# Kernel tuning notes

Measured on AMD Instinct MI355X. Metric: run time of the kernel, lower is better.

The kernel has to match this reference:

```python
import jax, jax.numpy as jnp
import numpy as np

DIM = 1024
B, S = 16, 2048

def setup_inputs() -> dict:
    key = jax.random.key(0)
    ks = jax.random.split(key, 8)
    scale = 1.0 / np.sqrt(DIM)
    x = jax.random.normal(ks[0], (B, S, DIM), dtype=jnp.float32)
    mask = jax.random.randint(ks[1], (B, S), 0, 2, dtype=jnp.int32)
    Wq = jax.random.normal(ks[2], (DIM, DIM), dtype=jnp.float32) * scale
    Wk = jax.random.normal(ks[3], (DIM, DIM), dtype=jnp.float32) * scale
    Wv = jax.random.normal(ks[4], (DIM, DIM), dtype=jnp.float32) * scale
    bq = jax.random.normal(ks[5], (DIM,), dtype=jnp.float32) * 0.01
    bk = jax.random.normal(ks[6], (DIM,), dtype=jnp.float32) * 0.01
    bv = jax.random.normal(ks[7], (DIM,), dtype=jnp.float32) * 0.01
    return {"x": x, "mask": mask, "Wq": Wq, "bq": bq, "Wk": Wk, "bk": bk, "Wv": Wv, "bv": bv}

def reference(x, mask, Wq, bq, Wk, bk, Wv, bv):
    # Q/K/V projections (torch Linear: x @ W.T + b)
    Q = jnp.einsum('bsd,ed->bse', x, Wq) + bq
    K = jnp.einsum('bsd,ed->bse', x, Wk) + bk
    V = jnp.einsum('bsd,ed->bse', x, Wv) + bv
    inv_sqrt_d = 1.0 / jnp.sqrt(jnp.asarray(x.shape[-1], dtype=x.dtype))
    scores = jnp.einsum('bqd,bkd->bqk', Q, K) * inv_sqrt_d  # [B,S,S]
    # mask: [B,S] -> broadcast over query dim; 0 = padding -> -inf
    scores = jnp.where(mask[:, None, :] == 0, -jnp.inf, scores)
    attn = jax.nn.softmax(scores, axis=-1)
    attn = jnp.nan_to_num(attn, nan=0.0)  # rows fully masked -> 0 (matches torch)
    out = jnp.einsum('bqk,bkd->bqd', attn, V)
    return out.mean(axis=1)  # [B, DIM]
```

## Files before the change

kernel.cpp:

```cpp
#include <hip/hip_runtime.h>
#include <hip/hip_bf16.h>
#include <stdint.h>

#define NBATCH 16
#define SEQ    2048
#define DMODEL 1024
#define KSPLIT 16

#define CS      0.03125f
#define KSC     3.0517578125e-5f
#define NEG4LN2 2.772588722f

typedef __attribute__((ext_vector_type(8))) short short8;
typedef __attribute__((ext_vector_type(4))) float f32x4;
typedef __attribute__((ext_vector_type(4))) int i32x4;
typedef __attribute__((ext_vector_type(16))) int i32x16;

struct __align__(8) bf4 { __hip_bfloat16 h[4]; };

__device__ __forceinline__ float bf2f(short s) {
  union { uint32_t u; float f; } c;
  c.u = ((uint32_t)(uint16_t)s) << 16;
  return c.f;
}
__device__ __forceinline__ int qs8(float f, float sc) {
  int v = __float2int_rn(f * sc);
  return v > 127 ? 127 : (v < -127 ? -127 : v);
}

__device__ __forceinline__ void gload16(const void* g, void* l) {
  __builtin_amdgcn_global_load_lds(
      (const __attribute__((address_space(1))) void*)g,
      (__attribute__((address_space(3))) void*)l, 16, 0, 0);
}

#define BAR() __builtin_amdgcn_s_barrier()
#define WAIT_LGKM0()                                         \
  do {                                                       \
    asm volatile("s_waitcnt lgkmcnt(0)" ::: "memory");       \
    __builtin_amdgcn_sched_barrier(0);                       \
  } while (0)
#define WAIT_VM0()                                           \
  do {                                                       \
    asm volatile("s_waitcnt vmcnt(0)" ::: "memory");         \
  } while (0)

template <int TP>
__global__ __launch_bounds__(512, 2)
void gemmT_kernel(const __hip_bfloat16* __restrict__ Aall,
                  const __hip_bfloat16* __restrict__ Ball,
                  uint8_t* __restrict__ O8, int ldo) {
  __shared__ __align__(16) char smem[131072];
  const int t = threadIdx.x, lane = t & 63, wid = t >> 6;
  const int wm = wid >> 2, wn = wid & 3;
  const int g = lane >> 4, l15 = lane & 15, l7 = lane & 7;

  const int at2base = blockIdx.x * TP;
  const int bt2 = blockIdx.y;
  const __hip_bfloat16* Bb = Ball + (size_t)bt2 * 256 * DMODEL;
  auto Aof = [&](int tp) { return Aall + (size_t)(at2base + tp) * 256 * DMODEL; };

  const int srl = t >> 3;
  const int sc8 = (t & 7) ^ (srl & 7);
  const int pc8[2] = {g ^ l7, (4 + g) ^ l7};

  auto stage_mat = [&](const __hip_bfloat16* gs, char* dst, int kt) {
#pragma unroll
    for (int it = 0; it < 4; ++it)
      gload16(gs + (size_t)(it * 64 + srl) * DMODEL + kt * 64 + sc8 * 8,
              dst + it * 8192 + wid * 1024);
  };

  f32x4 acc[8][4];
#pragma unroll
  for (int m = 0; m < 8; ++m)
#pragma unroll
    for (int n = 0; n < 4; ++n) acc[m][n] = (f32x4){0.f, 0.f, 0.f, 0.f};
  short8 afr[2][4], bfr[2][2][2];

#define LDA_Q(MH)                                                           \
  { _Pragma("unroll") for (int m = 0; m < 4; ++m) {                         \
      const int row = wm * 128 + ((MH) * 4 + m) * 16 + l15;                 \
      afr[0][m] = *(const short8*)(At + row * 128 + pc8[0] * 16);           \
      afr[1][m] = *(const short8*)(At + row * 128 + pc8[1] * 16);           \
    } }
#define LDB_Q(NH)                                                           \
  { _Pragma("unroll") for (int n = 0; n < 2; ++n) {                         \
      const int row = wn * 64 + ((NH) * 2 + n) * 16 + l15;                  \
      bfr[NH][0][n] = *(const short8*)(Bt + row * 128 + pc8[0] * 16);       \
      bfr[NH][1][n] = *(const short8*)(Bt + row * 128 + pc8[1] * 16);       \
    } }
#define MFMA_Q(MH, NH)                                                      \
  { __builtin_amdgcn_s_setprio(1);                                          \
    _Pragma("unroll") for (int kk = 0; kk < 2; ++kk)                        \
    _Pragma("unroll") for (int m = 0; m < 4; ++m)                           \
    _Pragma("unroll") for (int n = 0; n < 2; ++n)                           \
      acc[(MH)*4+m][(NH)*2+n] = __builtin_amdgcn_mfma_f32_16x16x32_bf16(    \
          afr[kk][m], bfr[NH][kk][n], acc[(MH)*4+m][(NH)*2+n], 0, 0, 0);    \
    __builtin_amdgcn_s_setprio(0); }

  auto EPI = [&](int at2) {
    const size_t orow0 = (size_t)bt2 * 256 + wn * 64 + l15;
    const int ocol0 = at2 * 256 + wm * 128 + g * 4;
#pragma unroll
    for (int mi = 0; mi < 8; ++mi)
#pragma unroll
      for (int ni = 0; ni < 4; ++ni) {
        uint32_t pk = 0;
#pragma unroll
        for (int j = 0; j < 4; ++j)
          pk |= (uint32_t)(qs8(acc[mi][ni][j], 1024.f) & 0xff) << (8 * j);
        *(uint32_t*)(O8 + (orow0 + ni * 16) * (size_t)ldo + ocol0 + mi * 16) = pk;
      }
#pragma unroll
    for (int m = 0; m < 8; ++m)
#pragma unroll
      for (int n = 0; n < 4; ++n) acc[m][n] = (f32x4){0.f, 0.f, 0.f, 0.f};
  };

  stage_mat(Aof(0), smem, 0);
  stage_mat(Bb, smem + 32768, 0);
  WAIT_VM0();
  BAR();

  const int NI = 16 * TP;
#pragma unroll 1
  for (int ii = 0; ii < NI; ++ii) {
    const int p = ii & 1;
    const char* At = smem + (p << 16);
    const char* Bt = smem + 32768 + (p << 16);
    char* An = smem + ((p ^ 1) << 16);
    char* Bn = smem + 32768 + ((p ^ 1) << 16);
    const int kn = (ii + 1) & 15;
    LDA_Q(0) LDB_Q(0)
    if (ii + 1 < NI) stage_mat(Aof((ii + 1) >> 4), An, kn);
    BAR(); WAIT_LGKM0(); MFMA_Q(0, 0) BAR();
    LDB_Q(1)
    if (ii + 1 < NI) stage_mat(Bb, Bn, kn);
    BAR(); WAIT_LGKM0(); MFMA_Q(0, 1) BAR();
    LDA_Q(1)
    BAR(); WAIT_LGKM0(); MFMA_Q(1, 0) BAR();
    MFMA_Q(1, 1)
    WAIT_VM0();
    if ((ii & 15) == 15) EPI(at2base + (ii >> 4));
    BAR();
  }
#undef LDA_Q
#undef LDB_Q
#undef MFMA_Q
}

template <int MODE, int TP>
__global__ __launch_bounds__(1024)
void i8gemm_kernel(const uint8_t* __restrict__ Aall,
                   const uint8_t* __restrict__ Ball,
                   uint8_t* __restrict__ OUT8,
                   const float* __restrict__ vball,
                   float* __restrict__ Zpart, int b0) {
  __shared__ __align__(16) char smem[131072 + 4096];
  const int t = threadIdx.x, lane = t & 63, wid = t >> 6;
  const int wm = wid >> 2, wn = wid & 3;
  const int l31 = lane & 31, half = lane >> 5, l7 = lane & 7;

  int at2base, bt2, cb = 0, b = 0;
  const uint8_t *Bb, *Abatch;
  if constexpr (MODE == 0) {
    at2base = blockIdx.x * TP;
    bt2 = blockIdx.y;
    Abatch = Aall;
    Bb = Ball + (size_t)bt2 * 256 * DMODEL;
  } else {
    cb = blockIdx.y; b = b0 + cb;
    bt2 = blockIdx.x & 7;
    at2base = (blockIdx.x >> 3) * TP;
    Abatch = Aall + (size_t)b * SEQ * DMODEL;
    Bb = Ball + ((size_t)b * SEQ + bt2 * 256) * DMODEL;
  }
  auto Aof = [&](int tp) { return Abatch + (size_t)(at2base + tp) * 256 * DMODEL; };

  const int sc8 = (t & 7) ^ ((t >> 3) & 7);
  int pcI[4];
#pragma unroll
  for (int ks = 0; ks < 4; ++ks) pcI[ks] = ((ks * 2 + half) ^ l7) * 16;

  auto stage_mat = [&](const uint8_t* gs, char* dst, int kt) {
#pragma unroll
    for (int it = 0; it < 2; ++it)
      gload16(gs + (size_t)(it * 128 + (t >> 3)) * DMODEL + kt * 128 + sc8 * 16,
              dst + it * 16384 + wid * 1024);
  };

  i32x16 acci[2][2];
#pragma unroll
  for (int m = 0; m < 2; ++m)
#pragma unroll
    for (int n = 0; n < 2; ++n)
#pragma unroll
      for (int r = 0; r < 16; ++r) acci[m][n][r] = 0;

  auto EPI = [&](int at2) {
    if constexpr (MODE == 0) {
#pragma unroll
      for (int mt = 0; mt < 2; ++mt) {
        const int arow_base = at2 * 256 + wm * 64 + mt * 32 + 4 * half;
#pragma unroll
        for (int nt = 0; nt < 2; ++nt) {
          const int bcol = bt2 * 256 + wn * 64 + nt * 32 + l31;
#pragma unroll
          for (int r = 0; r < 16; ++r) {
            const int arow = arow_base + (r & 3) + 8 * (r >> 2);
            OUT8[(size_t)arow * DMODEL + bcol] =
                (uint8_t)qs8((float)acci[mt][nt][r], 9.765625e-4f);
          }
        }
      }
    } else {
      float zc[2] = {0.f, 0.f};
#pragma unroll
      for (int mt = 0; mt < 2; ++mt) {
        const int krow_base = at2 * 256 + wm * 64 + mt * 32 + 4 * half;
        float4 vv[4];
#pragma unroll
        for (int gg = 0; gg < 4; ++gg)
          vv[gg] = *(const float4*)&vball[(size_t)b * SEQ + krow_base + 8 * gg];
#pragma unroll
        for (int nt = 0; nt < 2; ++nt) {
          const int qcol = bt2 * 256 + wn * 64 + nt * 32 + l31;
#pragma unroll
          for (int r = 0; r < 16; r += 2) {
            const float vj0 = ((const float*)&vv[r >> 2])[r & 3];
            const float vj1 = ((const float*)&vv[r >> 2])[(r + 1) & 3];
            const float e0 = __expf(fmaf((float)acci[mt][nt][r], KSC, vj0));
            const float e1 = __expf(fmaf((float)acci[mt][nt][r + 1], KSC, vj1));
            zc[nt] += e0 + e1;
            const unsigned p = __builtin_amdgcn_cvt_pk_fp8_f32(e0, e1, 0, false);
            const int krow = krow_base + (r & 3) + 8 * (r >> 2);
            uint8_t* ad = OUT8 + ((size_t)cb * SEQ + krow) * (size_t)SEQ + qcol;
            ad[0] = (uint8_t)p;
            ad[SEQ] = (uint8_t)(p >> 8);
          }
        }
      }
#pragma unroll
      for (int nt = 0; nt < 2; ++nt) {
        float v = zc[nt];
        v += __shfl_xor(v, 32);
        zc[nt] = v;
      }
      float* red = (float*)(smem + 131072);
      if (lane < 32) {
#pragma unroll
        for (int nt = 0; nt < 2; ++nt)
          red[wm * 256 + wn * 64 + nt * 32 + l31] = zc[nt];
      }
      __syncthreads();
      if (t < 256)
        Zpart[((size_t)cb * 8 + at2) * SEQ + bt2 * 256 + t] =
            red[t] + red[256 + t] + red[512 + t] + red[768 + t];
    }
#pragma unroll
    for (int m = 0; m < 2; ++m)
#pragma unroll
      for (int n = 0; n < 2; ++n)
#pragma unroll
        for (int r = 0; r < 16; ++r) acci[m][n][r] = 0;
  };

  stage_mat(Aof(0), smem, 0);
  stage_mat(Bb, smem + 32768, 0);
  WAIT_VM0();
  BAR();

  const int NI = 8 * TP;
#pragma unroll 1
  for (int ii = 0; ii < NI; ++ii) {
    const int p = ii & 1;
    const char* Al = smem + (p << 16);
    const char* Bl = smem + 32768 + (p << 16);
    if (ii + 1 < NI) {
      stage_mat(Aof((ii + 1) >> 3), smem + ((p ^ 1) << 16), (ii + 1) & 7);
      stage_mat(Bb, smem + 32768 + ((p ^ 1) << 16), (ii + 1) & 7);
    }
    const int rA0 = (wm * 64 + l31) * 128, rA1 = (wm * 64 + 32 + l31) * 128;
    const int rB0 = (wn * 64 + l31) * 128, rB1 = (wn * 64 + 32 + l31) * 128;
#pragma unroll
    for (int ks = 0; ks < 4; ++ks) {
      const i32x4 af0 = *(const i32x4*)(Al + rA0 + pcI[ks]);
      const i32x4 af1 = *(const i32x4*)(Al + rA1 + pcI[ks]);
      const i32x4 bf0 = *(const i32x4*)(Bl + rB0 + pcI[ks]);
      const i32x4 bf1 = *(const i32x4*)(Bl + rB1 + pcI[ks]);
      __builtin_amdgcn_s_setprio(1);
      acci[0][0] = __builtin_amdgcn_mfma_i32_32x32x32_i8(af0, bf0, acci[0][0], 0, 0, 0);
      acci[0][1] = __builtin_amdgcn_mfma_i32_32x32x32_i8(af0, bf1, acci[0][1], 0, 0, 0);
      acci[1][0] = __builtin_amdgcn_mfma_i32_32x32x32_i8(af1, bf0, acci[1][0], 0, 0, 0);
      acci[1][1] = __builtin_amdgcn_mfma_i32_32x32x32_i8(af1, bf1, acci[1][1], 0, 0, 0);
      __builtin_amdgcn_s_setprio(0);
    }
    WAIT_LGKM0();
    WAIT_VM0();
    if ((ii & 7) == 7) EPI(at2base + (ii >> 3));
    BAR();
  }
}

__global__ void transpose_cvt_kernel(const float* __restrict__ in,
                                     __hip_bfloat16* __restrict__ outp) {
  __shared__ float tile[32][33];
  const int bx = blockIdx.x, by = blockIdx.y;
  const int tx = threadIdx.x & 31, ty = threadIdx.x >> 5;
#pragma unroll
  for (int r = 0; r < 32; r += 8)
    tile[ty + r][tx] = in[(size_t)(by * 32 + ty + r) * DMODEL + bx * 32 + tx];
  __syncthreads();
#pragma unroll
  for (int r = 0; r < 32; r += 8)
    outp[(size_t)(bx * 32 + ty + r) * DMODEL + by * 32 + tx] =
        __float2bfloat16(tile[tx][ty + r]);
}

__global__ __launch_bounds__(256)
void prep_t2_kernel(const __hip_bfloat16* __restrict__ WkT,
                    const float* __restrict__ bq, float* __restrict__ t2) {
  const int wave = threadIdx.x >> 6, lane = threadIdx.x & 63;
  const int d = blockIdx.x * 4 + wave;
  const short8* kr = (const short8*)(WkT + (size_t)d * DMODEL);
  float a2 = 0.f;
#pragma unroll
  for (int h = 0; h < 2; ++h) {
    const short8 kv = kr[lane * 2 + h];
    const int e0 = lane * 16 + h * 8;
#pragma unroll
    for (int i = 0; i < 8; ++i) a2 += bf2f(kv[i]) * bq[e0 + i];
  }
  a2 += __shfl_down(a2, 32); a2 += __shfl_down(a2, 16); a2 += __shfl_down(a2, 8);
  a2 += __shfl_down(a2, 4);  a2 += __shfl_down(a2, 2);  a2 += __shfl_down(a2, 1);
  if (lane == 0) t2[d] = a2;
}

__global__ __launch_bounds__(256)
void cvtv_kernel(const float* __restrict__ x, const float* __restrict__ t2,
                 const int* __restrict__ mask,
                 uint8_t* __restrict__ x8, float* __restrict__ vb) {
  const int wave = threadIdx.x >> 6, lane = threadIdx.x & 63;
  const size_t row = (size_t)blockIdx.x * 4 + wave;
  const float* xr = x + row * DMODEL;
  float a2 = 0.f;
#pragma unroll
  for (int p = 0; p < 4; ++p) {
    const int d = p * 256 + lane * 4;
    const float4 xv = *(const float4*)(xr + d);
    const float4 tv = *(const float4*)(t2 + d);
    a2 += xv.x * tv.x + xv.y * tv.y + xv.z * tv.z + xv.w * tv.w;
    uint32_t qp = (uint32_t)(qs8(xv.x, 32.f) & 0xff) |
                  ((uint32_t)(qs8(xv.y, 32.f) & 0xff) << 8) |
                  ((uint32_t)(qs8(xv.z, 32.f) & 0xff) << 16) |
                  ((uint32_t)(qs8(xv.w, 32.f) & 0xff) << 24);
    *(uint32_t*)(x8 + row * DMODEL + d) = qp;
  }
  a2 += __shfl_down(a2, 32); a2 += __shfl_down(a2, 16); a2 += __shfl_down(a2, 8);
  a2 += __shfl_down(a2, 4);  a2 += __shfl_down(a2, 2);  a2 += __shfl_down(a2, 1);
  if (lane == 0)
    vb[row] = mask[row] ? fmaf(a2, CS, -NEG4LN2) : -1e30f;
}

__global__ void zinv_kernel(const float* __restrict__ Zpart,
                            float* __restrict__ rZ, int n) {
  const int idx = blockIdx.x * 256 + threadIdx.x;
  if (idx >= n) return;
  const int cb = idx >> 11, q = idx & (SEQ - 1);
  float z = 0.f;
#pragma unroll
  for (int kt = 0; kt < 8; ++kt)
    z += Zpart[((size_t)cb * 8 + kt) * SEQ + q];
  rZ[(size_t)cb * SEQ + q] = (z > 0.f) ? (1.f / z) : 0.f;
}

__global__ __launch_bounds__(256)
void passB_kernel(const uint8_t* __restrict__ E8,
                  const float* __restrict__ rZ,
                  float* __restrict__ wout) {
  const int t = threadIdx.x, lane = t & 63, wave = t >> 6;
  const int cb = blockIdx.y;
  float4 rzv[4][2];
#pragma unroll
  for (int it = 0; it < 4; ++it) {
    const float4* p = (const float4*)(rZ + (size_t)cb * SEQ + it * 512 + lane * 8);
    rzv[it][0] = p[0];
    rzv[it][1] = p[1];
  }
  const int kbase = blockIdx.x * 16 + wave * 4;
#pragma unroll
  for (int r = 0; r < 4; ++r) {
    const int k = kbase + r;
    const uint2* Ep = (const uint2*)(E8 + ((size_t)cb * SEQ + k) * SEQ);
    float s = 0.f;
#pragma unroll
    for (int it = 0; it < 4; ++it) {
      const uint2 v = Ep[it * 64 + lane];
      const float* rz = (const float*)&rzv[it][0];
      s += __builtin_amdgcn_cvt_f32_fp8(v.x, 0) * rz[0];
      s += __builtin_amdgcn_cvt_f32_fp8(v.x, 1) * rz[1];
      s += __builtin_amdgcn_cvt_f32_fp8(v.x, 2) * rz[2];
      s += __builtin_amdgcn_cvt_f32_fp8(v.x, 3) * rz[3];
      s += __builtin_amdgcn_cvt_f32_fp8(v.y, 0) * rz[4];
      s += __builtin_amdgcn_cvt_f32_fp8(v.y, 1) * rz[5];
      s += __builtin_amdgcn_cvt_f32_fp8(v.y, 2) * rz[6];
      s += __builtin_amdgcn_cvt_f32_fp8(v.y, 3) * rz[7];
    }
    s += __shfl_down(s, 32); s += __shfl_down(s, 16); s += __shfl_down(s, 8);
    s += __shfl_down(s, 4);  s += __shfl_down(s, 2);  s += __shfl_down(s, 1);
    if (lane == 0) wout[(size_t)cb * SEQ + k] = s;
  }
}

__global__ void sumw_kernel(const float* __restrict__ w,
                            float* __restrict__ sumw_all, int b0) {
  __shared__ float sred[4];
  const int t = threadIdx.x, lane = t & 63, wave = t >> 6;
  const int cb = blockIdx.x;
  float v = 0.f;
  for (int k = t; k < SEQ; k += 256) v += w[(size_t)cb * SEQ + k];
  v += __shfl_down(v, 32); v += __shfl_down(v, 16); v += __shfl_down(v, 8);
  v += __shfl_down(v, 4);  v += __shfl_down(v, 2);  v += __shfl_down(v, 1);
  if (lane == 0) sred[wave] = v;
  __syncthreads();
  if (t == 0) sumw_all[b0 + cb] = sred[0] + sred[1] + sred[2] + sred[3];
}

__global__ __launch_bounds__(256)
void wxpart_kernel(const uint8_t* __restrict__ x8,
                   const float* __restrict__ w,
                   float* __restrict__ wxp, int b0) {
  const int cb = blockIdx.y, kq = blockIdx.z;
  const int b = b0 + cb;
  const int d4 = threadIdx.x;
  const uint8_t* xb =
      x8 + ((size_t)b * SEQ + (size_t)kq * (SEQ / KSPLIT)) * DMODEL;
  const float* wb = w + (size_t)cb * SEQ + (size_t)kq * (SEQ / KSPLIT);
  float a0 = 0.f, a1 = 0.f, a2 = 0.f, a3 = 0.f;
#pragma unroll 4
  for (int k = 0; k < SEQ / KSPLIT; ++k) {
    const float wk = wb[k];
    const uint32_t pv = *(const uint32_t*)(xb + (size_t)k * DMODEL + d4 * 4);
    a0 += wk * (float)(int8_t)(pv & 0xff);
    a1 += wk * (float)(int8_t)((pv >> 8) & 0xff);
    a2 += wk * (float)(int8_t)((pv >> 16) & 0xff);
    a3 += wk * (float)(int8_t)(pv >> 24);
  }
  float4* o = (float4*)&wxp[((size_t)kq * NBATCH + b) * DMODEL + d4 * 4];
  *o = make_float4(a0 * 0.03125f, a1 * 0.03125f, a2 * 0.03125f, a3 * 0.03125f);
}

__global__ void final_kernel(const float* __restrict__ wxp,
                             const float* __restrict__ sumw_all,
                             const float* __restrict__ Wv,
                             const float* __restrict__ bv,
                             float* __restrict__ out) {
  const int b = blockIdx.y, eg = blockIdx.x;
  const int wave = threadIdx.x >> 6, lane = threadIdx.x & 63;
  const int e = eg * 4 + wave;
  float acc = 0.f;
  for (int d = lane; d < DMODEL; d += 64) {
    float wx = 0.f;
#pragma unroll
    for (int kq = 0; kq < KSPLIT; ++kq)
      wx += wxp[((size_t)kq * NBATCH + b) * DMODEL + d];
    acc += wx * Wv[(size_t)e * DMODEL + d];
  }
  acc += __shfl_down(acc, 32); acc += __shfl_down(acc, 16);
  acc += __shfl_down(acc, 8);  acc += __shfl_down(acc, 4);
  acc += __shfl_down(acc, 2);  acc += __shfl_down(acc, 1);
  if (lane == 0)
    out[(size_t)b * DMODEL + e] =
        (acc + sumw_all[b] * bv[e]) * (1.f / (float)SEQ);
}

extern "C" void kernel_launch(void* const* d_in, const int* in_sizes, int n_in,
                              void* d_out, int out_size, void* d_ws, size_t ws_size,
                              hipStream_t stream) {
  const float* x  = (const float*)d_in[0];
  const int* mask = (const int*)d_in[1];
  const float* Wq = (const float*)d_in[2];
  const float* bq = (const float*)d_in[3];
  const float* Wk = (const float*)d_in[4];
  const float* bk = (const float*)d_in[5];
  const float* Wv = (const float*)d_in[6];
  const float* bv = (const float*)d_in[7];
  float* out = (float*)d_out;
  (void)bk;

  char* ws = (char*)d_ws;
  size_t off = 0;
  auto alloc = [&](size_t bytes) -> void* {
    void* p = ws + off;
    off += (bytes + 255) & ~(size_t)255;
    return p;
  };
  uint8_t* Mt8 = (uint8_t*)alloc((size_t)DMODEL * DMODEL);
  __hip_bfloat16* WqT_bf = (__hip_bfloat16*)alloc((size_t)DMODEL * DMODEL * 2);
  __hip_bfloat16* WkT_bf = (__hip_bfloat16*)alloc((size_t)DMODEL * DMODEL * 2);
  float* wxp      = (float*)alloc((size_t)KSPLIT * NBATCH * DMODEL * 4);
  float* sumw_all = (float*)alloc((size_t)NBATCH * 4);
  float* t2       = (float*)alloc((size_t)DMODEL * 4);
  uint8_t* x8i = (uint8_t*)alloc((size_t)NBATCH * SEQ * DMODEL);
  uint8_t* Y8i = (uint8_t*)alloc((size_t)NBATCH * SEQ * DMODEL);
  float* vb = (float*)alloc((size_t)NBATCH * SEQ * 4);
  const size_t fixed = off;

  const size_t per_batch = (size_t)SEQ * SEQ
                         + (size_t)8 * SEQ * 4
                         + (size_t)2 * SEQ * 4 + 8 * 256;
  long avail = (long)ws_size - (long)fixed;
  int NB = (int)(avail / (long)per_batch);
  if (NB < 1) NB = 1;
  if (NB > NBATCH) NB = NBATCH;
  while (NBATCH % NB) --NB;
  uint8_t* Ebuf = (uint8_t*)alloc((size_t)NB * SEQ * SEQ);
  float* Zpart = (float*)alloc((size_t)NB * 8 * SEQ * 4);
  float* rZ    = (float*)alloc((size_t)NB * SEQ * 4);
  float* wbuf  = (float*)alloc((size_t)NB * SEQ * 4);

  transpose_cvt_kernel<<<dim3(32, 32), dim3(256), 0, stream>>>(Wq, WqT_bf);
  transpose_cvt_kernel<<<dim3(32, 32), dim3(256), 0, stream>>>(Wk, WkT_bf);
  gemmT_kernel<1><<<dim3(4, 4), dim3(512), 0, stream>>>(
      WqT_bf, WkT_bf, Mt8, DMODEL);
  prep_t2_kernel<<<dim3(256), dim3(256), 0, stream>>>(WkT_bf, bq, t2);
  cvtv_kernel<<<dim3(NBATCH * SEQ / 4), dim3(256), 0, stream>>>(
      x, t2, mask, x8i, vb);
  i8gemm_kernel<0, 2><<<dim3(64, DMODEL / 256), dim3(1024), 0, stream>>>(
      x8i, Mt8, Y8i, nullptr, nullptr, 0);

  for (int b0 = 0; b0 < NBATCH; b0 += NB) {
    const int nb = NB;
    i8gemm_kernel<1, 4><<<dim3(16, nb), dim3(1024), 0, stream>>>(
        x8i, Y8i, Ebuf, vb, Zpart, b0);
    zinv_kernel<<<dim3((nb * SEQ + 255) / 256), dim3(256), 0, stream>>>(
        Zpart, rZ, nb * SEQ);
    passB_kernel<<<dim3(SEQ / 16, nb), dim3(256), 0, stream>>>(Ebuf, rZ, wbuf);
    sumw_kernel<<<dim3(nb), dim3(256), 0, stream>>>(wbuf, sumw_all, b0);
    wxpart_kernel<<<dim3(1, nb, KSPLIT), dim3(256), 0, stream>>>(
        x8i, wbuf, wxp, b0);
  }
  final_kernel<<<dim3(DMODEL / 4, NBATCH), dim3(256), 0, stream>>>(
      wxp, sumw_all, Wv, bv, out);
}
```

Before: 277.6 us.

## Triple-buffer int8 GEMM staging and fuse softmax normalization kernels

```diff
diff --git a/kernel.cpp b/kernel.cpp
--- a/kernel.cpp
+++ b/kernel.cpp
@@ -43,6 +43,10 @@
 #define WAIT_VM0()                                           \
   do {                                                       \
     asm volatile("s_waitcnt vmcnt(0)" ::: "memory");         \
+  } while (0)
+#define WAIT_VM2()                                           \
+  do {                                                       \
+    asm volatile("s_waitcnt vmcnt(2)" ::: "memory");         \
   } while (0)
 
 template <int TP>
@@ -157,10 +161,10 @@
                    uint8_t* __restrict__ OUT8,
                    const float* __restrict__ vball,
                    float* __restrict__ Zpart, int b0) {
-  __shared__ __align__(16) char smem[131072 + 4096];
+  __shared__ __align__(16) char smem[98304 + 4096];
   const int t = threadIdx.x, lane = t & 63, wid = t >> 6;
   const int wm = wid >> 2, wn = wid & 3;
-  const int l31 = lane & 31, half = lane >> 5, l7 = lane & 7;
+  const int l31 = lane & 31, half = lane >> 5;
 
   int at2base, bt2, cb = 0, b = 0;
   const uint8_t *Bb, *Abatch;
@@ -178,17 +182,18 @@
   }
   auto Aof = [&](int tp) { return Abatch + (size_t)(at2base + tp) * 256 * DMODEL; };
 
-  const int sc8 = (t & 7) ^ ((t >> 3) & 7);
-  int pcI[4];
-#pragma unroll
-  for (int ks = 0; ks < 4; ++ks) pcI[ks] = ((ks * 2 + half) ^ l7) * 16;
-
-  auto stage_mat = [&](const uint8_t* gs, char* dst, int kt) {
-#pragma unroll
-    for (int it = 0; it < 2; ++it)
-      gload16(gs + (size_t)(it * 128 + (t >> 3)) * DMODEL + kt * 128 + sc8 * 16,
-              dst + it * 16384 + wid * 1024);
+  const int srow = t >> 2;
+  const int sc4 = (t & 3) ^ ((t >> 3) & 3);
+  auto stage_pair = [&](const uint8_t* ga, int kt, char* base) {
+    gload16(ga + (size_t)srow * DMODEL + kt * 64 + sc4 * 16, base + wid * 1024);
+    gload16(Bb + (size_t)srow * DMODEL + kt * 64 + sc4 * 16,
+            base + 16384 + wid * 1024);
   };
+
+  int pc4[2];
+#pragma unroll
+  for (int ks = 0; ks < 2; ++ks)
+    pc4[ks] = ((ks * 2 + half) ^ ((l31 >> 1) & 3)) * 16;
 
   i32x16 acci[2][2];
 #pragma unroll
@@ -247,7 +252,7 @@
         v += __shfl_xor(v, 32);
         zc[nt] = v;
       }
-      float* red = (float*)(smem + 131072);
+      float* red = (float*)(smem + 98304);
       if (lane < 32) {
 #pragma unroll
         for (int nt = 0; nt < 2; ++nt)
@@ -266,29 +271,27 @@
         for (int r = 0; r < 16; ++r) acci[m][n][r] = 0;
   };
 
-  stage_mat(Aof(0), smem, 0);
-  stage_mat(Bb, smem + 32768, 0);
-  WAIT_VM0();
+  const int NI = 16 * TP;
+  stage_pair(Aof(0), 0, smem);
+  if (NI > 1) stage_pair(Aof(1 >> 4), 1, smem + 32768);
+  WAIT_VM2();
   BAR();
 
-  const int NI = 8 * TP;
 #pragma unroll 1
-  for (int ii = 0; ii < NI; ++ii) {
-    const int p = ii & 1;
-    const char* Al = smem + (p << 16);
-    const char* Bl = smem + 32768 + (p << 16);
-    if (ii + 1 < NI) {
-      stage_mat(Aof((ii + 1) >> 3), smem + ((p ^ 1) << 16), (ii + 1) & 7);
-      stage_mat(Bb, smem + 32768 + ((p ^ 1) << 16), (ii + 1) & 7);
-    }
-    const int rA0 = (wm * 64 + l31) * 128, rA1 = (wm * 64 + 32 + l31) * 128;
-    const int rB0 = (wn * 64 + l31) * 128, rB1 = (wn * 64 + 32 + l31) * 128;
-#pragma unroll
-    for (int ks = 0; ks < 4; ++ks) {
-      const i32x4 af0 = *(const i32x4*)(Al + rA0 + pcI[ks]);
-      const i32x4 af1 = *(const i32x4*)(Al + rA1 + pcI[ks]);
-      const i32x4 bf0 = *(const i32x4*)(Bl + rB0 + pcI[ks]);
-      const i32x4 bf1 = *(const i32x4*)(Bl + rB1 + pcI[ks]);
+  for (int j = 0; j < NI; ++j) {
+    char* bcur = smem + (j % 3) * 32768;
+    if (j + 2 < NI)
+      stage_pair(Aof((j + 2) >> 4), (j + 2) & 15, smem + ((j + 2) % 3) * 32768);
+    const int rA0 = (wm * 64 + l31) * 64, rA1 = (wm * 64 + 32 + l31) * 64;
+    const int rB0 = (wn * 64 + l31) * 64, rB1 = (wn * 64 + 32 + l31) * 64;
+    const char* Al = bcur;
+    const char* Bl = bcur + 16384;
+#pragma unroll
+    for (int ks = 0; ks < 2; ++ks) {
+      const i32x4 af0 = *(const i32x4*)(Al + rA0 + pc4[ks]);
+      const i32x4 af1 = *(const i32x4*)(Al + rA1 + pc4[ks]);
+      const i32x4 bf0 = *(const i32x4*)(Bl + rB0 + pc4[ks]);
+      const i32x4 bf1 = *(const i32x4*)(Bl + rB1 + pc4[ks]);
       __builtin_amdgcn_s_setprio(1);
       acci[0][0] = __builtin_amdgcn_mfma_i32_32x32x32_i8(af0, bf0, acci[0][0], 0, 0, 0);
       acci[0][1] = __builtin_amdgcn_mfma_i32_32x32x32_i8(af0, bf1, acci[0][1], 0, 0, 0);
@@ -297,15 +300,20 @@
       __builtin_amdgcn_s_setprio(0);
     }
     WAIT_LGKM0();
-    WAIT_VM0();
-    if ((ii & 7) == 7) EPI(at2base + (ii >> 3));
+    if (j + 2 < NI) { WAIT_VM2(); }
+    else           { WAIT_VM0(); }
+    if ((j & 15) == 15) EPI(at2base + (j >> 4));
     BAR();
   }
 }
 
-__global__ void transpose_cvt_kernel(const float* __restrict__ in,
-                                     __hip_bfloat16* __restrict__ outp) {
+__global__ void transpose_cvt_kernel(const float* __restrict__ inq,
+                                     const float* __restrict__ ink,
+                                     __hip_bfloat16* __restrict__ outq,
+                                     __hip_bfloat16* __restrict__ outk) {
   __shared__ float tile[32][33];
+  const float* in = blockIdx.z ? ink : inq;
+  __hip_bfloat16* outp = blockIdx.z ? outk : outq;
   const int bx = blockIdx.x, by = blockIdx.y;
   const int tx = threadIdx.x & 31, ty = threadIdx.x >> 5;
 #pragma unroll
@@ -363,68 +371,58 @@
     vb[row] = mask[row] ? fmaf(a2, CS, -NEG4LN2) : -1e30f;
 }
 
-__global__ void zinv_kernel(const float* __restrict__ Zpart,
-                            float* __restrict__ rZ, int n) {
-  const int idx = blockIdx.x * 256 + threadIdx.x;
-  if (idx >= n) return;
-  const int cb = idx >> 11, q = idx & (SEQ - 1);
-  float z = 0.f;
-#pragma unroll
-  for (int kt = 0; kt < 8; ++kt)
-    z += Zpart[((size_t)cb * 8 + kt) * SEQ + q];
-  rZ[(size_t)cb * SEQ + q] = (z > 0.f) ? (1.f / z) : 0.f;
-}
-
 __global__ __launch_bounds__(256)
-void passB_kernel(const uint8_t* __restrict__ E8,
-                  const float* __restrict__ rZ,
-                  float* __restrict__ wout) {
+void wsolve_kernel(const uint8_t* __restrict__ E8,
+                   const float* __restrict__ Zpart,
+                   float* __restrict__ wout, float* __restrict__ sumwp,
+                   int b0) {
+  __shared__ float rz[SEQ];
+  __shared__ float sred[4];
   const int t = threadIdx.x, lane = t & 63, wave = t >> 6;
   const int cb = blockIdx.y;
+  for (int q = t; q < SEQ; q += 256) {
+    float z = 0.f;
+#pragma unroll
+    for (int kt = 0; kt < 8; ++kt)
+      z += Zpart[((size_t)cb * 8 + kt) * SEQ + q];
+    rz[q] = (z > 0.f) ? (1.f / z) : 0.f;
+  }
+  __syncthreads();
   float4 rzv[4][2];
 #pragma unroll
   for (int it = 0; it < 4; ++it) {
-    const float4* p = (const float4*)(rZ + (size_t)cb * SEQ + it * 512 + lane * 8);
-    rzv[it][0] = p[0];
-    rzv[it][1] = p[1];
-  }
-  const int kbase = blockIdx.x * 16 + wave * 4;
-#pragma unroll
-  for (int r = 0; r < 4; ++r) {
+    rzv[it][0] = *(const float4*)&rz[it * 512 + lane * 8];
+    rzv[it][1] = *(const float4*)&rz[it * 512 + lane * 8 + 4];
+  }
+  const int kbase = blockIdx.x * 128 + wave * 32;
+  float wsum = 0.f;
+#pragma unroll 1
+  for (int r = 0; r < 32; ++r) {
     const int k = kbase + r;
     const uint2* Ep = (const uint2*)(E8 + ((size_t)cb * SEQ + k) * SEQ);
     float s = 0.f;
 #pragma unroll
     for (int it = 0; it < 4; ++it) {
       const uint2 v = Ep[it * 64 + lane];
-      const float* rz = (const float*)&rzv[it][0];
-      s += __builtin_amdgcn_cvt_f32_fp8(v.x, 0) * rz[0];
-      s += __builtin_amdgcn_cvt_f32_fp8(v.x, 1) * rz[1];
-      s += __builtin_amdgcn_cvt_f32_fp8(v.x, 2) * rz[2];
-      s += __builtin_amdgcn_cvt_f32_fp8(v.x, 3) * rz[3];
-      s += __builtin_amdgcn_cvt_f32_fp8(v.y, 0) * rz[4];
-      s += __builtin_amdgcn_cvt_f32_fp8(v.y, 1) * rz[5];
-      s += __builtin_amdgcn_cvt_f32_fp8(v.y, 2) * rz[6];
-      s += __builtin_amdgcn_cvt_f32_fp8(v.y, 3) * rz[7];
+      const float* rzp = (const float*)&rzv[it][0];
+      s += __builtin_amdgcn_cvt_f32_fp8(v.x, 0) * rzp[0];
+      s += __builtin_amdgcn_cvt_f32_fp8(v.x, 1) * rzp[1];
+      s += __builtin_amdgcn_cvt_f32_fp8(v.x, 2) * rzp[2];
+      s += __builtin_amdgcn_cvt_f32_fp8(v.x, 3) * rzp[3];
+      s += __builtin_amdgcn_cvt_f32_fp8(v.y, 0) * rzp[4];
+      s += __builtin_amdgcn_cvt_f32_fp8(v.y, 1) * rzp[5];
+      s += __builtin_amdgcn_cvt_f32_fp8(v.y, 2) * rzp[6];
+      s += __builtin_amdgcn_cvt_f32_fp8(v.y, 3) * rzp[7];
     }
     s += __shfl_down(s, 32); s += __shfl_down(s, 16); s += __shfl_down(s, 8);
     s += __shfl_down(s, 4);  s += __shfl_down(s, 2);  s += __shfl_down(s, 1);
-    if (lane == 0) wout[(size_t)cb * SEQ + k] = s;
-  }
-}
-
-__global__ void sumw_kernel(const float* __restrict__ w,
-                            float* __restrict__ sumw_all, int b0) {
-  __shared__ float sred[4];
-  const int t = threadIdx.x, lane = t & 63, wave = t >> 6;
-  const int cb = blockIdx.x;
-  float v = 0.f;
-  for (int k = t; k < SEQ; k += 256) v += w[(size_t)cb * SEQ + k];
-  v += __shfl_down(v, 32); v += __shfl_down(v, 16); v += __shfl_down(v, 8);
-  v += __shfl_down(v, 4);  v += __shfl_down(v, 2);  v += __shfl_down(v, 1);
-  if (lane == 0) sred[wave] = v;
+    if (lane == 0) { wout[(size_t)cb * SEQ + k] = s; wsum += s; }
+  }
+  if (lane == 0) sred[wave] = wsum;
   __syncthreads();
-  if (t == 0) sumw_all[b0 + cb] = sred[0] + sred[1] + sred[2] + sred[3];
+  if (t == 0)
+    sumwp[(b0 + cb) * 16 + blockIdx.x] =
+        sred[0] + sred[1] + sred[2] + sred[3];
 }
 
 __global__ __launch_bounds__(256)
@@ -452,7 +450,7 @@
 }
 
 __global__ void final_kernel(const float* __restrict__ wxp,
-                             const float* __restrict__ sumw_all,
+                             const float* __restrict__ sumwp,
                              const float* __restrict__ Wv,
                              const float* __restrict__ bv,
                              float* __restrict__ out) {
@@ -470,9 +468,12 @@
   acc += __shfl_down(acc, 32); acc += __shfl_down(acc, 16);
   acc += __shfl_down(acc, 8);  acc += __shfl_down(acc, 4);
   acc += __shfl_down(acc, 2);  acc += __shfl_down(acc, 1);
-  if (lane == 0)
-    out[(size_t)b * DMODEL + e] =
-        (acc + sumw_all[b] * bv[e]) * (1.f / (float)SEQ);
+  if (lane == 0) {
+    float sw = 0.f;
+#pragma unroll
+    for (int i = 0; i < 16; ++i) sw += sumwp[b * 16 + i];
+    out[(size_t)b * DMODEL + e] = (acc + sw * bv[e]) * (1.f / (float)SEQ);
+  }
 }
 
 extern "C" void kernel_launch(void* const* d_in, const int* in_sizes, int n_in,
@@ -499,9 +500,9 @@
   uint8_t* Mt8 = (uint8_t*)alloc((size_t)DMODEL * DMODEL);
   __hip_bfloat16* WqT_bf = (__hip_bfloat16*)alloc((size_t)DMODEL * DMODEL * 2);
   __hip_bfloat16* WkT_bf = (__hip_bfloat16*)alloc((size_t)DMODEL * DMODEL * 2);
-  float* wxp      = (float*)alloc((size_t)KSPLIT * NBATCH * DMODEL * 4);
-  float* sumw_all = (float*)alloc((size_t)NBATCH * 4);
-  float* t2       = (float*)alloc((size_t)DMODEL * 4);
+  float* wxp   = (float*)alloc((size_t)KSPLIT * NBATCH * DMODEL * 4);
+  float* sumwp = (float*)alloc((size_t)NBATCH * 16 * 4);
+  float* t2    = (float*)alloc((size_t)DMODEL * 4);
   uint8_t* x8i = (uint8_t*)alloc((size_t)NBATCH * SEQ * DMODEL);
   uint8_t* Y8i = (uint8_t*)alloc((size_t)NBATCH * SEQ * DMODEL);
   float* vb = (float*)alloc((size_t)NBATCH * SEQ * 4);
@@ -509,7 +510,7 @@
 
   const size_t per_batch = (size_t)SEQ * SEQ
                          + (size_t)8 * SEQ * 4
-                         + (size_t)2 * SEQ * 4 + 8 * 256;
+                         + (size_t)SEQ * 4 + 8 * 256;
   long avail = (long)ws_size - (long)fixed;
   int NB = (int)(avail / (long)per_batch);
   if (NB < 1) NB = 1;
@@ -517,11 +518,10 @@
   while (NBATCH % NB) --NB;
   uint8_t* Ebuf = (uint8_t*)alloc((size_t)NB * SEQ * SEQ);
   float* Zpart = (float*)alloc((size_t)NB * 8 * SEQ * 4);
-  float* rZ    = (float*)alloc((size_t)NB * SEQ * 4);
   float* wbuf  = (float*)alloc((size_t)NB * SEQ * 4);
 
-  transpose_cvt_kernel<<<dim3(32, 32), dim3(256), 0, stream>>>(Wq, WqT_bf);
-  transpose_cvt_kernel<<<dim3(32, 32), dim3(256), 0, stream>>>(Wk, WkT_bf);
+  transpose_cvt_kernel<<<dim3(32, 32, 2), dim3(256), 0, stream>>>(
+      Wq, Wk, WqT_bf, WkT_bf);
   gemmT_kernel<1><<<dim3(4, 4), dim3(512), 0, stream>>>(
       WqT_bf, WkT_bf, Mt8, DMODEL);
   prep_t2_kernel<<<dim3(256), dim3(256), 0, stream>>>(WkT_bf, bq, t2);
@@ -534,13 +534,11 @@
     const int nb = NB;
     i8gemm_kernel<1, 4><<<dim3(16, nb), dim3(1024), 0, stream>>>(
         x8i, Y8i, Ebuf, vb, Zpart, b0);
-    zinv_kernel<<<dim3((nb * SEQ + 255) / 256), dim3(256), 0, stream>>>(
-        Zpart, rZ, nb * SEQ);
-    passB_kernel<<<dim3(SEQ / 16, nb), dim3(256), 0, stream>>>(Ebuf, rZ, wbuf);
-    sumw_kernel<<<dim3(nb), dim3(256), 0, stream>>>(wbuf, sumw_all, b0);
+    wsolve_kernel<<<dim3(16, nb), dim3(256), 0, stream>>>(
+        Ebuf, Zpart, wbuf, sumwp, b0);
     wxpart_kernel<<<dim3(1, nb, KSPLIT), dim3(256), 0, stream>>>(
         x8i, wbuf, wxp, b0);
   }
   final_kernel<<<dim3(DMODEL / 4, NBATCH), dim3(256), 0, stream>>>(
-      wxp, sumw_all, Wv, bv, out);
-}
+      wxp, sumwp, Wv, bv, out);
+}
```

Result: slower. 289.5 us (+4.3%).
